# Kernel tuning notes

Hardware: AMD Instinct MI355X
Metric: run time of the kernel (lower is better)

Reference implementation:

```python
import jax, jax.numpy as jnp
from jax import lax
import numpy as np


def setup_inputs() -> dict:
    key = jax.random.key(0)
    ks = jax.random.split(key, 7)
    B, T, I, H, O = 8192, 512, 7, 7, 1
    s = 1.0 / np.sqrt(H)
    return {
        "x": jax.random.normal(ks[0], (B, T, I), dtype=jnp.float32),
        "W_ih": jax.random.normal(ks[1], (H, I), dtype=jnp.float32) * s,
        "W_hh": jax.random.normal(ks[2], (H, H), dtype=jnp.float32) * s,
        "b_ih": jax.random.normal(ks[3], (H,), dtype=jnp.float32) * s,
        "b_hh": jax.random.normal(ks[4], (H,), dtype=jnp.float32) * s,
        "W_fc": jax.random.normal(ks[5], (O, H), dtype=jnp.float32) * s,
        "b_fc": jax.random.normal(ks[6], (O,), dtype=jnp.float32) * s,
    }


def reference(x, W_ih, W_hh, b_ih, b_hh, W_fc, b_fc):
    # Vanilla tanh RNN: h_t = tanh(x_t W_ih^T + b_ih + h_{t-1} W_hh^T + b_hh)
    B, T, _ = x.shape
    H = W_hh.shape[0]
    # Precompute the input projection for all timesteps (one big GEMM).
    xp = jnp.einsum("bti,hi->bth", x, W_ih) + (b_ih + b_hh)  # [B,T,H]
    h0 = jnp.zeros((B, H), dtype=x.dtype)

    def step(h, xt):
        h = jnp.tanh(xt + h @ W_hh.T)
        return h, h

    hT, hs = lax.scan(step, h0, jnp.swapaxes(xp, 0, 1))  # hs: [T,B,H]
    out_seq = jnp.swapaxes(hs, 0, 1)  # [B,T,H]
    out = (jnp.einsum("bth,oh->bto", out_seq, W_fc) + b_fc).squeeze(-1)  # [B,T]
    hidden = hT[None]  # [1,B,H] matching torch's (num_layers, B, H)
    return (out, hidden)
```

## Files before the change

### kernel.cpp

```cpp
#include <hip/hip_runtime.h>
#include <stdint.h>


#define B_TOTAL 8192
#define T_STEPS 512

#define DPP_QUAD0 0x00
#define DPP_QUAD1 0x55
#define DPP_QUAD2 0xAA
#define DPP_QUAD3 0xFF
#define DPP_XOR1  0xB1
#define DPP_XOR2  0x4E
#define DPP_HM    0x141

template <int CTRL>
__device__ __forceinline__ float dpp_mov(float v) {
    int s = __float_as_int(v);
    return __int_as_float(__builtin_amdgcn_update_dpp(s, s, CTRL, 0xF, 0xF, true));
}

__device__ __forceinline__ float tanh_fast(float a) {
    float e = __builtin_amdgcn_exp2f(a * 2.8853900817779268f);
    float r = __builtin_amdgcn_rcpf(e + 1.0f);
    return __builtin_fmaf(-2.0f, r, 1.0f);
}

typedef float v4f __attribute__((ext_vector_type(4)));

struct XChunk { v4f v[14]; };

__device__ __forceinline__ void chunk_issue(XChunk& ch, const float* base) {
    #pragma unroll
    for (int i = 0; i < 14; ++i)
        asm volatile("global_load_dwordx4 %0, %1, off offset:%2"
                     : "=v"(ch.v[i]) : "v"(base), "i"(16 * i));
}

#define CHUNK_WAIT(ch, N)                                                     \
    asm volatile("s_waitcnt vmcnt(" #N ")"                                    \
        : "+v"((ch).v[0]), "+v"((ch).v[1]), "+v"((ch).v[2]), "+v"((ch).v[3]), \
          "+v"((ch).v[4]), "+v"((ch).v[5]), "+v"((ch).v[6]), "+v"((ch).v[7]), \
          "+v"((ch).v[8]), "+v"((ch).v[9]), "+v"((ch).v[10]),                 \
          "+v"((ch).v[11]), "+v"((ch).v[12]), "+v"((ch).v[13]))

__global__ __launch_bounds__(256, 1) void rnn_kernel(
    const float* __restrict__ x,
    const float* __restrict__ Wih,
    const float* __restrict__ Whh,
    const float* __restrict__ bih,
    const float* __restrict__ bhh,
    const float* __restrict__ Wfc,
    const float* __restrict__ bfc,
    float* __restrict__ out)
{
    const int tid  = threadIdx.x;
    const int k    = tid & 7;
    const int b    = blockIdx.x * 32 + (tid >> 3);
    const int quad = (tid >> 2) & 1;

    float wih[7];
    float wa[4], wb[4];
    float bias = 0.0f, wfc_own = 0.0f;
    {
        float whh_row[8];
        #pragma unroll
        for (int i = 0; i < 8; ++i) whh_row[i] = 0.0f;
        if (k < 7) {
            #pragma unroll
            for (int i = 0; i < 7; ++i) {
                wih[i] = Wih[k * 7 + i];
                whh_row[i] = Whh[k * 7 + i];
            }
            bias = bih[k] + bhh[k];
            wfc_own = Wfc[k];
        } else {
            #pragma unroll
            for (int i = 0; i < 7; ++i) wih[i] = 0.0f;
        }
        #pragma unroll
        for (int j = 0; j < 4; ++j) {
            wa[j] = quad ? whh_row[4 + j] : whh_row[j];
            wb[j] = quad ? whh_row[j]     : whh_row[4 + j];
        }
    }
    const float bfcv = bfc[0];

    const float* xrow = x + (size_t)b * (T_STEPS * 7);
    float* outp = out + (size_t)b * T_STEPS;

    float a0 = 0.f, a1 = 0.f, a2 = 0.f, a3 = 0.f;
    float b0 = 0.f, b1 = 0.f, b2 = 0.f, b3 = 0.f;

    XChunk A, B;
    chunk_issue(A, xrow);
    chunk_issue(B, xrow + 56);

    auto do_chunk = [&](XChunk& buf, int c, const float* reload) {
        float u[8];
        {
            float xv[56];
            #pragma unroll
            for (int i = 0; i < 14; ++i) {
                xv[4 * i + 0] = buf.v[i].x; xv[4 * i + 1] = buf.v[i].y;
                xv[4 * i + 2] = buf.v[i].z; xv[4 * i + 3] = buf.v[i].w;
            }
            #pragma unroll
            for (int s = 0; s < 8; ++s) {
                const float* xs = &xv[s * 7];
                float p01 = __builtin_fmaf(wih[1], xs[1], wih[0] * xs[0]);
                float p23 = __builtin_fmaf(wih[3], xs[3], wih[2] * xs[2]);
                float p45 = __builtin_fmaf(wih[5], xs[5], wih[4] * xs[4]);
                float p6b = __builtin_fmaf(wih[6], xs[6], bias);
                u[s] = (p01 + p23) + (p45 + p6b);
            }
        }
        if (reload) chunk_issue(buf, reload);
        float hs[8];
        #pragma unroll
        for (int s = 0; s < 8; ++s) {
            float p0 = __builtin_fmaf(wa[0], a0, u[s]);
            float p1 = __builtin_fmaf(wa[2], a2, wa[1] * a1);
            float p2 = __builtin_fmaf(wb[0], b0, wa[3] * a3);
            float p3 = __builtin_fmaf(wb[2], b2, wb[1] * b1);
            float p4 = wb[3] * b3;
            float acc = (p0 + p1) + (p2 + (p3 + p4));
            float hk = tanh_fast(acc);
            hs[s] = hk;
            a0 = dpp_mov<DPP_QUAD0>(hk);
            a1 = dpp_mov<DPP_QUAD1>(hk);
            a2 = dpp_mov<DPP_QUAD2>(hk);
            a3 = dpp_mov<DPP_QUAD3>(hk);
            b0 = dpp_mov<DPP_HM>(a0);
            b1 = dpp_mov<DPP_HM>(a1);
            b2 = dpp_mov<DPP_HM>(a2);
            b3 = dpp_mov<DPP_HM>(a3);
        }
        float o[8];
        #pragma unroll
        for (int s = 0; s < 8; ++s) {
            float v = wfc_own * hs[s];
            v += dpp_mov<DPP_XOR1>(v);
            v += dpp_mov<DPP_XOR2>(v);
            v += dpp_mov<DPP_HM>(v);
            o[s] = v + bfcv;
        }
        if (k == 7) {
            *(float4*)(outp + c * 8 + 0) = make_float4(o[0], o[1], o[2], o[3]);
            *(float4*)(outp + c * 8 + 4) = make_float4(o[4], o[5], o[6], o[7]);
        }
    };

    #pragma unroll 1
    for (int c = 0; c < 62; c += 2) {
        CHUNK_WAIT(A, 14);
        do_chunk(A, c, xrow + (c + 2) * 56);
        CHUNK_WAIT(B, 14);
        do_chunk(B, c + 1, xrow + (c + 3) * 56);
    }
    CHUNK_WAIT(A, 14);
    do_chunk(A, 62, nullptr);
    CHUNK_WAIT(B, 0);
    do_chunk(B, 63, nullptr);

    if (k < 7) {
        int kk = k & 3;
        float hv = (kk == 0) ? a0 : (kk == 1) ? a1 : (kk == 2) ? a2 : a3;
        out[(size_t)B_TOTAL * T_STEPS + (size_t)b * 7 + k] = hv;
    }
}

extern "C" void kernel_launch(void* const* d_in, const int* in_sizes, int n_in,
                              void* d_out, int out_size, void* d_ws, size_t ws_size,
                              hipStream_t stream) {
    const float* x   = (const float*)d_in[0];
    const float* Wih = (const float*)d_in[1];
    const float* Whh = (const float*)d_in[2];
    const float* bih = (const float*)d_in[3];
    const float* bhh = (const float*)d_in[4];
    const float* Wfc = (const float*)d_in[5];
    const float* bfc = (const float*)d_in[6];
    float* out = (float*)d_out;

    rnn_kernel<<<dim3(B_TOTAL / 32), dim3(256), 0, stream>>>(
        x, Wih, Whh, bih, bhh, Wfc, bfc, out);
}
```

Before: 203.2 us.

## Split RNN into producer and recurrence warps communicating through LDS

Each 512-thread block is split into two roles. Four waves run only the serial tanh recurrence. The other four waves load x, compute the input projection into double-buffered LDS, and emit the output projection from stored hidden states. The aim is to take load latency and the non-recurrent arithmetic off the critical recurrence path. In exchange it adds a block-wide barrier every 8 timesteps and LDS round-trips, and it drops the hand-written asm prefetch, so the producer waves now do synchronous loads inside each step.

```diff
diff --git a/kernel.cpp b/kernel.cpp
--- a/kernel.cpp
+++ b/kernel.cpp
@@ -25,25 +25,7 @@
     return __builtin_fmaf(-2.0f, r, 1.0f);
 }
 
-typedef float v4f __attribute__((ext_vector_type(4)));
-
-struct XChunk { v4f v[14]; };
-
-__device__ __forceinline__ void chunk_issue(XChunk& ch, const float* base) {
-    #pragma unroll
-    for (int i = 0; i < 14; ++i)
-        asm volatile("global_load_dwordx4 %0, %1, off offset:%2"
-                     : "=v"(ch.v[i]) : "v"(base), "i"(16 * i));
-}
-
-#define CHUNK_WAIT(ch, N)                                                     \
-    asm volatile("s_waitcnt vmcnt(" #N ")"                                    \
-        : "+v"((ch).v[0]), "+v"((ch).v[1]), "+v"((ch).v[2]), "+v"((ch).v[3]), \
-          "+v"((ch).v[4]), "+v"((ch).v[5]), "+v"((ch).v[6]), "+v"((ch).v[7]), \
-          "+v"((ch).v[8]), "+v"((ch).v[9]), "+v"((ch).v[10]),                 \
-          "+v"((ch).v[11]), "+v"((ch).v[12]), "+v"((ch).v[13]))
-
-__global__ __launch_bounds__(256, 1) void rnn_kernel(
+__global__ __launch_bounds__(512, 2) void rnn_kernel(
     const float* __restrict__ x,
     const float* __restrict__ Wih,
     const float* __restrict__ Whh,
@@ -53,88 +35,54 @@
     const float* __restrict__ bfc,
     float* __restrict__ out)
 {
-    const int tid  = threadIdx.x;
-    const int k    = tid & 7;
-    const int b    = blockIdx.x * 32 + (tid >> 3);
-    const int quad = (tid >> 2) & 1;
-
-    float wih[7];
-    float wa[4], wb[4];
-    float bias = 0.0f, wfc_own = 0.0f;
-    {
-        float whh_row[8];
-        #pragma unroll
-        for (int i = 0; i < 8; ++i) whh_row[i] = 0.0f;
-        if (k < 7) {
-            #pragma unroll
-            for (int i = 0; i < 7; ++i) {
-                wih[i] = Wih[k * 7 + i];
-                whh_row[i] = Whh[k * 7 + i];
-            }
-            bias = bih[k] + bhh[k];
-            wfc_own = Wfc[k];
-        } else {
-            #pragma unroll
-            for (int i = 0; i < 7; ++i) wih[i] = 0.0f;
-        }
-        #pragma unroll
-        for (int j = 0; j < 4; ++j) {
-            wa[j] = quad ? whh_row[4 + j] : whh_row[j];
-            wb[j] = quad ? whh_row[j]     : whh_row[4 + j];
-        }
-    }
-    const float bfcv = bfc[0];
-
+    const int tid   = threadIdx.x;
+    const int wid   = tid >> 6;
+    const int role  = wid >> 2;
+    const int pair  = wid & 3;
+    const int lane  = tid & 63;
+    const int k     = lane & 7;
+    const int b     = blockIdx.x * 32 + pair * 8 + (lane >> 3);
+    const int lbase = lane * 10;
+
+    __shared__ __attribute__((aligned(16))) float lds_u[2][4][640];
+    __shared__ __attribute__((aligned(16))) float lds_h[2][4][640];
+
+    float wa[4] = {0.f, 0.f, 0.f, 0.f}, wb[4] = {0.f, 0.f, 0.f, 0.f};
+    float ra0 = 0.f, ra1 = 0.f, ra2 = 0.f, ra3 = 0.f;
+    float rb0 = 0.f, rb1 = 0.f, rb2 = 0.f, rb3 = 0.f;
+    float wih[7] = {0.f, 0.f, 0.f, 0.f, 0.f, 0.f, 0.f};
+    float bias = 0.f, wfc_own = 0.f, bfcv = 0.f;
     const float* xrow = x + (size_t)b * (T_STEPS * 7);
     float* outp = out + (size_t)b * T_STEPS;
 
-    float a0 = 0.f, a1 = 0.f, a2 = 0.f, a3 = 0.f;
-    float b0 = 0.f, b1 = 0.f, b2 = 0.f, b3 = 0.f;
-
-    XChunk A, B;
-    chunk_issue(A, xrow);
-    chunk_issue(B, xrow + 56);
-
-    auto do_chunk = [&](XChunk& buf, int c, const float* reload) {
+    auto u_store = [&](const float4* xb, int par) {
+        float xv[56];
+        #pragma unroll
+        for (int i = 0; i < 14; ++i) {
+            xv[4 * i + 0] = xb[i].x; xv[4 * i + 1] = xb[i].y;
+            xv[4 * i + 2] = xb[i].z; xv[4 * i + 3] = xb[i].w;
+        }
         float u[8];
-        {
-            float xv[56];
-            #pragma unroll
-            for (int i = 0; i < 14; ++i) {
-                xv[4 * i + 0] = buf.v[i].x; xv[4 * i + 1] = buf.v[i].y;
-                xv[4 * i + 2] = buf.v[i].z; xv[4 * i + 3] = buf.v[i].w;
-            }
-            #pragma unroll
-            for (int s = 0; s < 8; ++s) {
-                const float* xs = &xv[s * 7];
-                float p01 = __builtin_fmaf(wih[1], xs[1], wih[0] * xs[0]);
-                float p23 = __builtin_fmaf(wih[3], xs[3], wih[2] * xs[2]);
-                float p45 = __builtin_fmaf(wih[5], xs[5], wih[4] * xs[4]);
-                float p6b = __builtin_fmaf(wih[6], xs[6], bias);
-                u[s] = (p01 + p23) + (p45 + p6b);
-            }
-        }
-        if (reload) chunk_issue(buf, reload);
-        float hs[8];
         #pragma unroll
         for (int s = 0; s < 8; ++s) {
-            float p0 = __builtin_fmaf(wa[0], a0, u[s]);
-            float p1 = __builtin_fmaf(wa[2], a2, wa[1] * a1);
-            float p2 = __builtin_fmaf(wb[0], b0, wa[3] * a3);
-            float p3 = __builtin_fmaf(wb[2], b2, wb[1] * b1);
-            float p4 = wb[3] * b3;
-            float acc = (p0 + p1) + (p2 + (p3 + p4));
-            float hk = tanh_fast(acc);
-            hs[s] = hk;
-            a0 = dpp_mov<DPP_QUAD0>(hk);
-            a1 = dpp_mov<DPP_QUAD1>(hk);
-            a2 = dpp_mov<DPP_QUAD2>(hk);
-            a3 = dpp_mov<DPP_QUAD3>(hk);
-            b0 = dpp_mov<DPP_HM>(a0);
-            b1 = dpp_mov<DPP_HM>(a1);
-            b2 = dpp_mov<DPP_HM>(a2);
-            b3 = dpp_mov<DPP_HM>(a3);
-        }
+            const float* xs = &xv[s * 7];
+            float p01 = __builtin_fmaf(wih[1], xs[1], wih[0] * xs[0]);
+            float p23 = __builtin_fmaf(wih[3], xs[3], wih[2] * xs[2]);
+            float p45 = __builtin_fmaf(wih[5], xs[5], wih[4] * xs[4]);
+            float p6b = __builtin_fmaf(wih[6], xs[6], bias);
+            u[s] = (p01 + p23) + (p45 + p6b);
+        }
+        float2* up = (float2*)&lds_u[par][pair][lbase];
+        up[0] = make_float2(u[0], u[1]);
+        up[1] = make_float2(u[2], u[3]);
+        up[2] = make_float2(u[4], u[5]);
+        up[3] = make_float2(u[6], u[7]);
+    };
+
+    auto emit_out = [&](int t) {
+        const float2* hp = (const float2*)&lds_h[t & 1][pair][lbase];
+        float2 h01 = hp[0], h23 = hp[1], h45 = hp[2], h67 = hp[3];
+        float hs[8] = {h01.x, h01.y, h23.x, h23.y, h45.x, h45.y, h67.x, h67.y};
         float o[8];
         #pragma unroll
         for (int s = 0; s < 8; ++s) {
@@ -145,27 +93,97 @@
             o[s] = v + bfcv;
         }
         if (k == 7) {
-            *(float4*)(outp + c * 8 + 0) = make_float4(o[0], o[1], o[2], o[3]);
-            *(float4*)(outp + c * 8 + 4) = make_float4(o[4], o[5], o[6], o[7]);
+            *(float4*)(outp + t * 8 + 0) = make_float4(o[0], o[1], o[2], o[3]);
+            *(float4*)(outp + t * 8 + 4) = make_float4(o[4], o[5], o[6], o[7]);
         }
     };
 
+    auto rec_step = [&](int par) {
+        const float2* up = (const float2*)&lds_u[par][pair][lbase];
+        float2 u01 = up[0], u23 = up[1], u45 = up[2], u67 = up[3];
+        float u[8] = {u01.x, u01.y, u23.x, u23.y, u45.x, u45.y, u67.x, u67.y};
+        float hs[8];
+        #pragma unroll
+        for (int s = 0; s < 8; ++s) {
+            float p0 = __builtin_fmaf(wa[0], ra0, u[s]);
+            float p1 = __builtin_fmaf(wa[2], ra2, wa[1] * ra1);
+            float p2 = __builtin_fmaf(wb[0], rb0, wa[3] * ra3);
+            float p3 = __builtin_fmaf(wb[2], rb2, wb[1] * rb1);
+            float p4 = wb[3] * rb3;
+            float acc = (p0 + p1) + (p2 + (p3 + p4));
+            float hk = tanh_fast(acc);
+            hs[s] = hk;
+            ra0 = dpp_mov<DPP_QUAD0>(hk);
+            ra1 = dpp_mov<DPP_QUAD1>(hk);
+            ra2 = dpp_mov<DPP_QUAD2>(hk);
+            ra3 = dpp_mov<DPP_QUAD3>(hk);
+            rb0 = dpp_mov<DPP_HM>(ra0);
+            rb1 = dpp_mov<DPP_HM>(ra1);
+            rb2 = dpp_mov<DPP_HM>(ra2);
+            rb3 = dpp_mov<DPP_HM>(ra3);
+        }
+        float2* hp = (float2*)&lds_h[par][pair][lbase];
+        hp[0] = make_float2(hs[0], hs[1]);
+        hp[1] = make_float2(hs[2], hs[3]);
+        hp[2] = make_float2(hs[4], hs[5]);
+        hp[3] = make_float2(hs[6], hs[7]);
+    };
+
+    if (role == 0) {
+        const int quad = (lane >> 2) & 1;
+        float whh_row[8];
+        #pragma unroll
+        for (int i = 0; i < 8; ++i) whh_row[i] = 0.0f;
+        if (k < 7) {
+            #pragma unroll
+            for (int i = 0; i < 7; ++i) whh_row[i] = Whh[k * 7 + i];
+        }
+        #pragma unroll
+        for (int j = 0; j < 4; ++j) {
+            wa[j] = quad ? whh_row[4 + j] : whh_row[j];
+            wb[j] = quad ? whh_row[j]     : whh_row[4 + j];
+        }
+    } else {
+        if (k < 7) {
+            #pragma unroll
+            for (int i = 0; i < 7; ++i) wih[i] = Wih[k * 7 + i];
+            bias = bih[k] + bhh[k];
+            wfc_own = Wfc[k];
+        }
+        bfcv = bfc[0];
+        float4 xb[14];
+        const float4* src = (const float4*)xrow;
+        #pragma unroll
+        for (int i = 0; i < 14; ++i) xb[i] = src[i];
+        u_store(xb, 0);
+    }
+    __syncthreads();
+
     #pragma unroll 1
-    for (int c = 0; c < 62; c += 2) {
-        CHUNK_WAIT(A, 14);
-        do_chunk(A, c, xrow + (c + 2) * 56);
-        CHUNK_WAIT(B, 14);
-        do_chunk(B, c + 1, xrow + (c + 3) * 56);
+    for (int t = 0; t < 64; ++t) {
+        if (role == 0) {
+            rec_step(t & 1);
+        } else {
+            float4 xb[14];
+            if (t < 63) {
+                const float4* src = (const float4*)(xrow + (t + 1) * 56);
+                #pragma unroll
+                for (int i = 0; i < 14; ++i) xb[i] = src[i];
+            }
+            if (t > 0) emit_out(t - 1);
+            if (t < 63) u_store(xb, (t + 1) & 1);
+        }
+        __syncthreads();
     }
-    CHUNK_WAIT(A, 14);
-    do_chunk(A, 62, nullptr);
-    CHUNK_WAIT(B, 0);
-    do_chunk(B, 63, nullptr);
-
-    if (k < 7) {
-        int kk = k & 3;
-        float hv = (kk == 0) ? a0 : (kk == 1) ? a1 : (kk == 2) ? a2 : a3;
-        out[(size_t)B_TOTAL * T_STEPS + (size_t)b * 7 + k] = hv;
+
+    if (role == 0) {
+        if (k < 7) {
+            int kk = k & 3;
+            float hv = (kk == 0) ? ra0 : (kk == 1) ? ra1 : (kk == 2) ? ra2 : ra3;
+            out[(size_t)B_TOTAL * T_STEPS + (size_t)b * 7 + k] = hv;
+        }
+    } else {
+        emit_out(63);
     }
 }
 
@@ -181,6 +199,6 @@
     const float* bfc = (const float*)d_in[6];
     float* out = (float*)d_out;
 
-    rnn_kernel<<<dim3(B_TOTAL / 32), dim3(256), 0, stream>>>(
+    rnn_kernel<<<dim3(B_TOTAL / 32), dim3(512), 0, stream>>>(
         x, Wih, Whh, bih, bhh, Wfc, bfc, out);
 }
```

Result: slower. 240.9 us (+18.6%).
